# Performance work log

Hardware: AMD Instinct MI355X
Metric: run time of the kernel (lower is better)

The kernel has to match this reference:

```python
import jax, jax.numpy as jnp
import numpy as np

Q_MAX = 127.0  # int8 symmetric quant range
EPS = 1e-7

def setup_inputs() -> dict:
    key = jax.random.key(0)
    k1, k2, k3, k4 = jax.random.split(key, 4)
    M, K, N = 8192, 4096, 4096
    x = jax.random.normal(k1, (M, K), dtype=jnp.float32)
    # int8 weight stored as int32 for portability; values in [-127, 127]
    weight_i8 = jax.random.randint(k2, (N, K), -127, 128, dtype=jnp.int32)
    # per-output-channel weight scale (small positive)
    w_scale = jax.random.uniform(k3, (N,), dtype=jnp.float32) * 0.01 + 1e-4
    bias = jax.random.normal(k4, (N,), dtype=jnp.float32)
    return {"x": x, "weight_i8": weight_i8, "w_scale": w_scale, "bias": bias}

def reference(x, weight_i8, w_scale, bias):
    # per-token dynamic symmetric quantization of activations
    absmax = jnp.max(jnp.abs(x), axis=-1, keepdims=True)            # [M, 1]
    x_scale = jnp.maximum(absmax, EPS) / Q_MAX                       # [M, 1]
    x_q = jnp.clip(jnp.round(x / x_scale), -Q_MAX, Q_MAX)            # [M, K] int values in fp32
    acc = jnp.einsum('mk,nk->mn', x_q, weight_i8.astype(jnp.float32))  # [M, N]
    out = acc * x_scale * w_scale[None, :] + bias[None, :]
    return out
```

## Files before the change

kernel.cpp:

```cpp
#include <hip/hip_runtime.h>
#include <stdint.h>

#define Q_MAX_F 127.0f
#define EPS_F 1e-7f

typedef int   v4i __attribute__((ext_vector_type(4)));
typedef float v4f __attribute__((ext_vector_type(4)));

__global__ __launch_bounds__(256) void quant_x_kernel(
    const float* __restrict__ x, int8_t* __restrict__ xq,
    float* __restrict__ xscale, int K) {
  const int row = blockIdx.x;
  const int t = threadIdx.x;
  const float* xr = x + (size_t)row * K;

  float v[16];
  float m = 0.f;
#pragma unroll
  for (int c = 0; c < 4; ++c) {
    v4f f = *(const v4f*)(xr + c * 1024 + t * 4);
#pragma unroll
    for (int j = 0; j < 4; ++j) {
      v[c * 4 + j] = f[j];
      m = fmaxf(m, fabsf(f[j]));
    }
  }
#pragma unroll
  for (int off = 32; off; off >>= 1) m = fmaxf(m, __shfl_xor(m, off));
  __shared__ float sm[4];
  if ((t & 63) == 0) sm[t >> 6] = m;
  __syncthreads();
  m = fmaxf(fmaxf(sm[0], sm[1]), fmaxf(sm[2], sm[3]));

  const float s = fmaxf(m, EPS_F) / Q_MAX_F;
  if (t == 0) xscale[row] = s;

  int* xqi = (int*)xq;
#pragma unroll
  for (int c = 0; c < 4; ++c) {
    int packed = 0;
#pragma unroll
    for (int j = 0; j < 4; ++j) {
      float q = rintf(v[c * 4 + j] / s);
      q = fminf(fmaxf(q, -127.f), 127.f);
      int qi = (int)q;
      packed |= (qi & 0xff) << (8 * j);
    }
    xqi[(size_t)row * (K / 4) + c * 256 + t] = packed;
  }
}

__global__ __launch_bounds__(256) void pack_w_kernel(
    const int* __restrict__ w, int8_t* __restrict__ wq, long n4) {
  long i = (long)blockIdx.x * 256 + threadIdx.x;
  if (i >= n4) return;
  v4i a = ((const v4i*)w)[i];
  int packed = (a[0] & 0xff) | ((a[1] & 0xff) << 8) |
               ((a[2] & 0xff) << 16) | ((a[3] & 0xff) << 24);
  ((int*)wq)[i] = packed;
}

#define BM 128
#define BN 128
#define BKB 64

__global__ __launch_bounds__(256) void w8a8_gemm_kernel(
    const int8_t* __restrict__ xq, const int8_t* __restrict__ wq,
    const float* __restrict__ xscale, const float* __restrict__ wscale,
    const float* __restrict__ bias, float* __restrict__ out,
    int M, int N, int K) {
  __shared__ __align__(16) char lds[2][2 * BM * BKB];

  const int t = threadIdx.x;
  const int lane = t & 63;
  const int wid = t >> 6;

  const int nwg = gridDim.x;
  int bid = blockIdx.x;
  int wg = ((nwg & 7) == 0) ? ((bid & 7) * (nwg >> 3) + (bid >> 3)) : bid;

  const int nbn = N / BN;
  const int bm = (wg / nbn) * BM;
  const int bn = (wg % nbn) * BN;

  const int wm = (wid >> 1) * 64;
  const int wn = (wid & 1) * 64;

  v4i acc[4][4] = {};

  const char* gA = (const char*)xq + (size_t)bm * K;
  const char* gB = (const char*)wq + (size_t)bn * K;

  auto stage = [&](char* buf, int k0) {
#pragma unroll
    for (int j = 0; j < 4; ++j) {
      const int q = wid * 4 + j;
      const int part = q >> 3;
      const int qq = q & 7;
      const int lin = qq * 1024 + lane * 16;
      const int row = lin >> 6;
      const int cp = (lin >> 4) & 3;
      const int c = cp ^ ((row >> 1) & 3);
      const char* src = (part ? gB : gA) + (size_t)row * K + k0 + c * 16;
      char* dst = buf + part * 8192 + qq * 1024;
      __builtin_amdgcn_global_load_lds(
          (const __attribute__((address_space(1))) void*)src,
          (__attribute__((address_space(3))) void*)dst, 16, 0, 0);
    }
  };

  const int NT = K / BKB;
  int cur = 0;
  stage(lds[0], 0);
  __syncthreads();

  for (int tk = 0; tk < NT; ++tk) {
    if (tk + 1 < NT) stage(lds[cur ^ 1], (tk + 1) * BKB);

    const char* bufA = lds[cur];
    const char* bufB = lds[cur] + 8192;
    const int chunk = lane >> 4;
    const int rl = lane & 15;

    v4i a[4], b[4];
#pragma unroll
    for (int i = 0; i < 4; ++i) {
      int row = wm + i * 16 + rl;
      int addr = row * 64 + ((chunk ^ ((row >> 1) & 3)) << 4);
      a[i] = *(const v4i*)(bufA + addr);
    }
#pragma unroll
    for (int i = 0; i < 4; ++i) {
      int row = wn + i * 16 + rl;
      int addr = row * 64 + ((chunk ^ ((row >> 1) & 3)) << 4);
      b[i] = *(const v4i*)(bufB + addr);
    }
#pragma unroll
    for (int i = 0; i < 4; ++i)
#pragma unroll
      for (int j = 0; j < 4; ++j)
        acc[i][j] = __builtin_amdgcn_mfma_i32_16x16x64_i8(a[i], b[j], acc[i][j], 0, 0, 0);

    __syncthreads();
    cur ^= 1;
  }

  const int r0 = (lane >> 4) * 4;
  const int cn = lane & 15;
#pragma unroll
  for (int i = 0; i < 4; ++i) {
    const int growb = bm + wm + i * 16 + r0;
#pragma unroll
    for (int j = 0; j < 4; ++j) {
      const int gcol = bn + wn + j * 16 + cn;
      const float wsc = wscale[gcol];
      const float bs = bias[gcol];
#pragma unroll
      for (int r = 0; r < 4; ++r) {
        const int grow = growb + r;
        const float xs = xscale[grow];
        out[(size_t)grow * N + gcol] = (float)acc[i][j][r] * (xs * wsc) + bs;
      }
    }
  }
}

extern "C" void kernel_launch(void* const* d_in, const int* in_sizes, int n_in,
                              void* d_out, int out_size, void* d_ws, size_t ws_size,
                              hipStream_t stream) {
  const float* x = (const float*)d_in[0];
  const int* w = (const int*)d_in[1];
  const float* wscale = (const float*)d_in[2];
  const float* bias = (const float*)d_in[3];
  float* out = (float*)d_out;

  const int N = in_sizes[2];
  const long wk = (long)in_sizes[1];
  const int K = (int)(wk / N);
  const int M = (int)((long)in_sizes[0] / K);

  int8_t* xq = (int8_t*)d_ws;
  int8_t* wq = xq + (size_t)M * K;
  float* xscale = (float*)(wq + (size_t)N * K);

  quant_x_kernel<<<M, 256, 0, stream>>>(x, xq, xscale, K);

  const long n4 = (long)N * K / 4;
  pack_w_kernel<<<(int)((n4 + 255) / 256), 256, 0, stream>>>(w, wq, n4);

  const int nwg = (M / BM) * (N / BN);
  w8a8_gemm_kernel<<<nwg, 256, 0, stream>>>(xq, wq, xscale, wscale, bias, out,
                                            M, N, K);
}
```

Baseline: 444.6 us.

## Enlarge GEMM tile to 256x256 with 4-stage LDS pipeline and split barriers

The GEMM moves to 256x256 workgroup tiles with 8 waves and a 4-deep ring of 128 KB dynamic LDS buffers filled by async global-to-LDS loads. Each K step is split into two halves with staged prefetches, explicit vmcnt waits, setprio around the MFMA blocks, and raw s_barrier instead of __syncthreads. The aim is more data reuse per byte loaded and better overlap of memory with MFMA. The quant kernel also replaces its division with a reciprocal multiply. The cost is higher register pressure, and at 128 KB of LDS per block the launch_bounds occupancy hint of 2 may not be reachable. Only 512 workgroups run, and the reciprocal multiply can round differently from a true division.

```diff
diff --git a/kernel.cpp b/kernel.cpp
--- a/kernel.cpp
+++ b/kernel.cpp
@@ -33,6 +33,7 @@
   m = fmaxf(fmaxf(sm[0], sm[1]), fmaxf(sm[2], sm[3]));
 
   const float s = fmaxf(m, EPS_F) / Q_MAX_F;
+  const float inv = 1.0f / s;
   if (t == 0) xscale[row] = s;
 
   int* xqi = (int*)xq;
@@ -41,10 +42,9 @@
     int packed = 0;
 #pragma unroll
     for (int j = 0; j < 4; ++j) {
-      float q = rintf(v[c * 4 + j] / s);
+      float q = rintf(v[c * 4 + j] * inv);
       q = fminf(fmaxf(q, -127.f), 127.f);
-      int qi = (int)q;
-      packed |= (qi & 0xff) << (8 * j);
+      packed |= ((int)q & 0xff) << (8 * j);
     }
     xqi[(size_t)row * (K / 4) + c * 256 + t] = packed;
   }
@@ -60,20 +60,21 @@
   ((int*)wq)[i] = packed;
 }
 
-#define BM 128
-#define BN 128
-#define BKB 64
-
-__global__ __launch_bounds__(256) void w8a8_gemm_kernel(
+#define BM 256
+#define BN 256
+
+__global__ __launch_bounds__(512, 2) void w8a8_gemm_kernel(
     const int8_t* __restrict__ xq, const int8_t* __restrict__ wq,
     const float* __restrict__ xscale, const float* __restrict__ wscale,
     const float* __restrict__ bias, float* __restrict__ out,
     int M, int N, int K) {
-  __shared__ __align__(16) char lds[2][2 * BM * BKB];
+  extern __shared__ char lds[];
 
   const int t = threadIdx.x;
   const int lane = t & 63;
   const int wid = t >> 6;
+  const int wr = wid >> 2;
+  const int wc = wid & 3;
 
   const int nwg = gridDim.x;
   int bid = blockIdx.x;
@@ -83,76 +84,88 @@
   const int bm = (wg / nbn) * BM;
   const int bn = (wg % nbn) * BN;
 
-  const int wm = (wid >> 1) * 64;
-  const int wn = (wid & 1) * 64;
-
-  v4i acc[4][4] = {};
-
   const char* gA = (const char*)xq + (size_t)bm * K;
   const char* gB = (const char*)wq + (size_t)bn * K;
 
-  auto stage = [&](char* buf, int k0) {
-#pragma unroll
-    for (int j = 0; j < 4; ++j) {
-      const int q = wid * 4 + j;
-      const int part = q >> 3;
-      const int qq = q & 7;
-      const int lin = qq * 1024 + lane * 16;
+  v4i acc[8][4] = {};
+
+  auto stage_part = [&](int kt, int p) {
+    const char* gsrc = p ? gB : gA;
+    char* dstbase = lds + (size_t)(kt & 3) * 32768 + p * 16384;
+#pragma unroll
+    for (int i = 0; i < 2; ++i) {
+      const int lin = i * 8192 + wid * 1024 + lane * 16;
       const int row = lin >> 6;
-      const int cp = (lin >> 4) & 3;
-      const int c = cp ^ ((row >> 1) & 3);
-      const char* src = (part ? gB : gA) + (size_t)row * K + k0 + c * 16;
-      char* dst = buf + part * 8192 + qq * 1024;
+      const int cs = (lane & 3) ^ ((row >> 1) & 3);
+      const char* src = gsrc + (size_t)row * K + kt * 64 + cs * 16;
       __builtin_amdgcn_global_load_lds(
           (const __attribute__((address_space(1))) void*)src,
-          (__attribute__((address_space(3))) void*)dst, 16, 0, 0);
+          (__attribute__((address_space(3))) void*)(dstbase + i * 8192 + wid * 1024),
+          16, 0, 0);
     }
   };
 
-  const int NT = K / BKB;
-  int cur = 0;
-  stage(lds[0], 0);
-  __syncthreads();
-
-  for (int tk = 0; tk < NT; ++tk) {
-    if (tk + 1 < NT) stage(lds[cur ^ 1], (tk + 1) * BKB);
-
-    const char* bufA = lds[cur];
-    const char* bufB = lds[cur] + 8192;
-    const int chunk = lane >> 4;
-    const int rl = lane & 15;
-
-    v4i a[4], b[4];
+  const int NT = K / 64;
+  const int rl = lane & 15;
+  const int ck = lane >> 4;
+
+  for (int kt = 0; kt < 3; ++kt) { stage_part(kt, 0); stage_part(kt, 1); }
+  asm volatile("s_waitcnt vmcnt(8)" ::: "memory");
+  asm volatile("s_barrier" ::: "memory");
+
+  for (int kt = 0; kt < NT; ++kt) {
+    const char* bufA = lds + (size_t)(kt & 3) * 32768;
+    const char* bufB = bufA + 16384;
+
+    v4i b[4], a[4];
+#pragma unroll
+    for (int j = 0; j < 4; ++j) {
+      const int r = wc * 64 + j * 16 + rl;
+      b[j] = *(const v4i*)(bufB + r * 64 + ((ck ^ ((r >> 1) & 3)) << 4));
+    }
 #pragma unroll
     for (int i = 0; i < 4; ++i) {
-      int row = wm + i * 16 + rl;
-      int addr = row * 64 + ((chunk ^ ((row >> 1) & 3)) << 4);
-      a[i] = *(const v4i*)(bufA + addr);
-    }
-#pragma unroll
-    for (int i = 0; i < 4; ++i) {
-      int row = wn + i * 16 + rl;
-      int addr = row * 64 + ((chunk ^ ((row >> 1) & 3)) << 4);
-      b[i] = *(const v4i*)(bufB + addr);
-    }
+      const int r = wr * 128 + i * 16 + rl;
+      a[i] = *(const v4i*)(bufA + r * 64 + ((ck ^ ((r >> 1) & 3)) << 4));
+    }
+    if (kt + 3 < NT) stage_part(kt + 3, 0);
+    __builtin_amdgcn_s_setprio(1);
 #pragma unroll
     for (int i = 0; i < 4; ++i)
 #pragma unroll
       for (int j = 0; j < 4; ++j)
         acc[i][j] = __builtin_amdgcn_mfma_i32_16x16x64_i8(a[i], b[j], acc[i][j], 0, 0, 0);
-
-    __syncthreads();
-    cur ^= 1;
+    __builtin_amdgcn_s_setprio(0);
+    asm volatile("s_barrier" ::: "memory");
+
+#pragma unroll
+    for (int i = 0; i < 4; ++i) {
+      const int r = wr * 128 + 64 + i * 16 + rl;
+      a[i] = *(const v4i*)(bufA + r * 64 + ((ck ^ ((r >> 1) & 3)) << 4));
+    }
+    if (kt + 3 < NT) stage_part(kt + 3, 1);
+    __builtin_amdgcn_s_setprio(1);
+#pragma unroll
+    for (int i = 0; i < 4; ++i)
+#pragma unroll
+      for (int j = 0; j < 4; ++j)
+        acc[4 + i][j] = __builtin_amdgcn_mfma_i32_16x16x64_i8(a[i], b[j], acc[4 + i][j], 0, 0, 0);
+    __builtin_amdgcn_s_setprio(0);
+
+    if (kt <= NT - 4)      asm volatile("s_waitcnt vmcnt(8)" ::: "memory");
+    else if (kt == NT - 3) asm volatile("s_waitcnt vmcnt(4)" ::: "memory");
+    else if (kt == NT - 2) asm volatile("s_waitcnt vmcnt(0)" ::: "memory");
+    asm volatile("s_barrier" ::: "memory");
   }
 
   const int r0 = (lane >> 4) * 4;
   const int cn = lane & 15;
 #pragma unroll
-  for (int i = 0; i < 4; ++i) {
-    const int growb = bm + wm + i * 16 + r0;
-#pragma unroll
-    for (int j = 0; j < 4; ++j) {
-      const int gcol = bn + wn + j * 16 + cn;
+  for (int i = 0; i < 8; ++i) {
+    const int growb = bm + wr * 128 + i * 16 + r0;
+#pragma unroll
+    for (int j = 0; j < 4; ++j) {
+      const int gcol = bn + wc * 64 + j * 16 + cn;
       const float wsc = wscale[gcol];
       const float bs = bias[gcol];
 #pragma unroll
@@ -189,6 +202,6 @@
   pack_w_kernel<<<(int)((n4 + 255) / 256), 256, 0, stream>>>(w, wq, n4);
 
   const int nwg = (M / BM) * (N / BN);
-  w8a8_gemm_kernel<<<nwg, 256, 0, stream>>>(xq, wq, xscale, wscale, bias, out,
-                                            M, N, K);
-}
+  w8a8_gemm_kernel<<<nwg, 512, 131072, stream>>>(xq, wq, xscale, wscale, bias,
+                                                 out, M, N, K);
+}
```

Measured after the change: 398.7 us. -10.3%, faster.
